# Kernel optimization log

Hardware: AMD Instinct MI355X
Metric: run time of the kernel (lower is better)

## Reference

```python
import jax, jax.numpy as jnp
import numpy as np

B, S, D, H, RANK, NC = 2, 2048, 1024, 16, 128, 16
DH = D // H


def setup_inputs() -> dict:
    key = jax.random.key(0)
    ks = jax.random.split(key, 10)
    x = jax.random.normal(ks[0], (B, S, D), jnp.float32)
    # causal mask, broadcast over batch and heads like torch's [B,1,S,S]
    mask = jnp.tril(jnp.ones((S, S), dtype=bool))[None, None]
    # orthogonal-ish init approximated by scaled gaussian
    compress_neurons = jax.random.normal(ks[1], (NC, D, RANK), jnp.float32) / np.sqrt(D)
    router_Q = jax.random.normal(ks[2], (NC, D), jnp.float32) * 0.02
    router_K = jax.random.normal(ks[3], (NC, D), jnp.float32) * 0.02
    router_V = jax.random.normal(ks[4], (NC, D), jnp.float32) * 0.02
    wQ = jax.random.normal(ks[5], (D, RANK), jnp.float32) / np.sqrt(RANK)
    wK = jax.random.normal(ks[6], (D, RANK), jnp.float32) / np.sqrt(RANK)
    wV = jax.random.normal(ks[7], (D, RANK), jnp.float32) / np.sqrt(RANK)
    wO = jax.random.normal(ks[8], (D, D), jnp.float32) / np.sqrt(D)
    return {"x": x, "mask": mask, "compress_neurons": compress_neurons,
            "router_Q": router_Q, "router_K": router_K, "router_V": router_V,
            "wQ": wQ, "wK": wK, "wV": wV, "wO": wO}


def reference(x, mask, compress_neurons, router_Q, router_K, router_V, wQ, wK, wV, wO):
    def compress(router_w):
        # router scores -> softmax over all n_compress neurons
        w = jax.nn.softmax(jnp.einsum('bsd,nd->bsn', x, router_w), axis=-1)  # [B,S,NC]
        # softmax-weighted sum of all neuron projections (fused einsum)
        return jnp.einsum('bsd,ndr,bsn->bsr', x, compress_neurons, w)  # [B,S,RANK]

    hQ = compress(router_Q)
    hK = compress(router_K)
    hV = compress(router_V)
    # expand rank -> d_model (Linear weight [D,RANK]), then split heads
    Q = jnp.einsum('bsr,dr->bsd', hQ, wQ).reshape(B, S, H, DH).transpose(0, 2, 1, 3)
    K = jnp.einsum('bsr,dr->bsd', hK, wK).reshape(B, S, H, DH).transpose(0, 2, 1, 3)
    V = jnp.einsum('bsr,dr->bsd', hV, wV).reshape(B, S, H, DH).transpose(0, 2, 1, 3)
    scores = jnp.einsum('bhqd,bhkd->bhqk', Q, K) / np.sqrt(DH)  # [B,H,S,S]
    scores = jnp.where(mask, scores, -jnp.inf)
    attn = jax.nn.softmax(scores, axis=-1)
    attn_out = jnp.einsum('bhqk,bhkd->bhqd', attn, V)
    attn_out = attn_out.transpose(0, 2, 1, 3).reshape(B, S, D)
    # dropout omitted (eval mode / dropout=0)
    return jnp.einsum('bsd,ed->bse', attn_out, wO)
```

## Files before the change

### kernel.cpp

```cpp
#include <hip/hip_runtime.h>
#include <hip/hip_bf16.h>
#include <math.h>

#define B_ 2
#define S_ 2048
#define D_ 1024
#define H_ 16
#define RANK_ 128
#define NC_ 16
#define DH_ 64
#define T_ (B_*S_)
#define NZ_ 2176

typedef __attribute__((ext_vector_type(8))) __bf16 bf16x8;
typedef __attribute__((ext_vector_type(8))) unsigned short u16x8;
typedef __attribute__((ext_vector_type(4))) float f32x4;
typedef __attribute__((ext_vector_type(16))) float f32x16;

#if __has_builtin(__builtin_amdgcn_exp2f)
#define EXP2F(x) __builtin_amdgcn_exp2f(x)
#else
#define EXP2F(x) exp2f(x)
#endif

__device__ __forceinline__ unsigned short f2bu(float f) {
    __hip_bfloat16 h = __float2bfloat16(f);
    unsigned short u; __builtin_memcpy(&u, &h, 2); return u;
}
__device__ __forceinline__ float bu2f(unsigned short u) {
    __hip_bfloat16 h; __builtin_memcpy(&h, &u, 2); return __bfloat162float(h);
}

__device__ __forceinline__ void gl_lds16(const unsigned short* g, unsigned short* l) {
    __builtin_amdgcn_global_load_lds(
        (const __attribute__((address_space(1))) void*)g,
        (__attribute__((address_space(3))) void*)l, 16, 0, 0);
}

__device__ __forceinline__ unsigned cvtpk_bf16(float lo, float hi) {
    unsigned r;
    asm("v_cvt_pk_bf16_f32 %0, %1, %2" : "=v"(r) : "v"(lo), "v"(hi));
    return r;
}
__device__ __forceinline__ void plswap(unsigned &a, unsigned &b) {
    asm("v_permlane32_swap_b32 %0, %1" : "+v"(a), "+v"(b));
}

__device__ __forceinline__ bool sniff_f32(const unsigned* __restrict__ p) {
    int votes = 0;
    #pragma unroll
    for (int i = 0; i < 64; i++) {
        unsigned e = (p[i] >> 23) & 0xFFu;
        votes += (e >= 0x60u && e <= 0x8Fu) ? 1 : 0;
    }
    return votes >= 32;
}

struct Cvt { const void* src[9]; unsigned short* dst[9]; const void* C; unsigned short* Ct; };

__global__ __launch_bounds__(256) void k_inputs(Cvt cv,
    const unsigned* __restrict__ probe)
{
    bool f32 = sniff_f32(probe);
    if (blockIdx.x < 512) {
        int bid = blockIdx.x;
        int d0 = (bid & 15) * 64, r0 = ((bid >> 4) & 1) * 64, n = bid >> 5;
        __shared__ unsigned short tile[64][65];
        for (int idx = threadIdx.x; idx < 4096; idx += 256) {
            int row = idx >> 6, col = idx & 63;
            size_t si = ((size_t)n*D_ + d0 + row)*RANK_ + r0 + col;
            tile[row][col] = f32 ? f2bu(((const float*)cv.C)[si])
                                 : ((const unsigned short*)cv.C)[si];
        }
        __syncthreads();
        for (int idx = threadIdx.x; idx < 4096; idx += 256) {
            int row = idx >> 6, col = idx & 63;
            cv.Ct[((size_t)(n*RANK_ + r0 + row))*D_ + d0 + col] = tile[col][row];
        }
        return;
    }
    const int offs[9] = {0, 4194304, 4210688, 4227072, 4243456,
                         4259840, 4390912, 4521984, 4653056};
    const int total = 5701632;
    int nconv = gridDim.x - 512;
    int stride = nconv * 256;
    for (int i = (blockIdx.x - 512) * 256 + threadIdx.x; i < total; i += stride) {
        int seg = 0;
        #pragma unroll
        for (int s = 1; s < 9; s++) seg += (i >= offs[s]) ? 1 : 0;
        int local = i - offs[seg];
        const void* sp = cv.src[seg];
        unsigned short v = 0;
        if (sp) v = f32 ? f2bu(((const float*)sp)[local]) : ((const unsigned short*)sp)[local];
        cv.dst[seg][local] = v;
    }
}

template<int MT, int MODE>
__global__ __launch_bounds__(256) void k_mfma_gemm(const unsigned short* __restrict__ A,
    const unsigned short* __restrict__ Bm, void* __restrict__ Cout,
    const unsigned* __restrict__ probe, int M, int N, int K)
{
    bool f32out = false;
    if (MODE == 2) f32out = sniff_f32(probe);
    __shared__ __align__(16) unsigned short As[MT*32*32];
    __shared__ __align__(16) unsigned short Bs[128*32];
    const int tid = threadIdx.x;
    const int wv = tid >> 6, lane = tid & 63;
    const int wm = (wv >> 1) * (MT*16), wn = (wv & 1) * 64;
    const int quad = lane >> 4, l16 = lane & 15;
    const int m0 = blockIdx.x * (MT*32), n0 = blockIdx.y * 128;

    const f32x4 z4 = {0.f, 0.f, 0.f, 0.f};
    f32x4 acc[MT][4];
    #pragma unroll
    for (int i = 0; i < MT; i++)
        #pragma unroll
        for (int j = 0; j < 4; j++) acc[i][j] = z4;

    for (int k0 = 0; k0 < K; k0 += 32) {
        __syncthreads();
        #pragma unroll
        for (int c = 0; c < MT/2; c++) {
            int idx = wv*64 + c*256 + lane;
            gl_lds16(A + (size_t)(m0 + (idx >> 2))*K + k0 + (idx & 3)*8,
                     &As[(wv*64 + c*256)*8]);
        }
        #pragma unroll
        for (int c = 0; c < 2; c++) {
            int idx = wv*64 + c*256 + lane;
            gl_lds16(Bm + (size_t)(n0 + (idx >> 2))*K + k0 + (idx & 3)*8,
                     &Bs[(wv*64 + c*256)*8]);
        }
        __syncthreads();
        bf16x8 af[MT], bfr[4];
        #pragma unroll
        for (int mt = 0; mt < MT; mt++) af[mt]  = *(const bf16x8*)&As[(wm + mt*16 + l16)*32 + quad*8];
        #pragma unroll
        for (int nt = 0; nt < 4; nt++) bfr[nt] = *(const bf16x8*)&Bs[(wn + nt*16 + l16)*32 + quad*8];
        #pragma unroll
        for (int mt = 0; mt < MT; mt++)
            #pragma unroll
            for (int nt = 0; nt < 4; nt++)
                acc[mt][nt] = __builtin_amdgcn_mfma_f32_16x16x32_bf16(af[mt], bfr[nt], acc[mt][nt], 0, 0, 0);
    }
    #pragma unroll
    for (int mt = 0; mt < MT; mt++)
        #pragma unroll
        for (int nt = 0; nt < 4; nt++) {
            int col = n0 + wn + nt*16 + l16;
            #pragma unroll
            for (int r = 0; r < 4; r++) {
                int rowg = m0 + wm + mt*16 + quad*4 + r;
                float v = acc[mt][nt][r];
                if (MODE == 2 && f32out) ((float*)Cout)[(size_t)rowg*N + col] = v;
                else  ((unsigned short*)Cout)[(size_t)rowg*N + col] = f2bu(v);
            }
        }
}

__global__ __launch_bounds__(256) void k_qkv2(const unsigned short* __restrict__ h3,
    const unsigned short* __restrict__ wqkv, unsigned short* __restrict__ QKb,
    unsigned short* __restrict__ Vtg)
{
    __shared__ __align__(16) unsigned short As[128*32];
    __shared__ __align__(16) unsigned short Bs[128*32];
    const int tid = threadIdx.x;
    const int wv = tid >> 6, lane = tid & 63;
    const int wm = (wv >> 1) * 64, wn = (wv & 1) * 64;
    const int quad = lane >> 4, l16 = lane & 15;

    const bool vt = (blockIdx.x >= 512);
    int m0, n0;
    const unsigned short *A, *Bm;
    float scale = 1.f;
    if (!vt) {
        int id = blockIdx.x;
        m0 = (id & 31) * 128;
        n0 = (id >> 5) * 128;
        int w = n0 >> 10;
        A  = h3 + (size_t)w * T_ * RANK_ + (size_t)m0 * RANK_;
        Bm = wqkv + (size_t)w * D_ * RANK_ + (size_t)(n0 & 1023) * RANK_;
        if (w == 0) scale = 0.125f * 1.44269504f;
    } else {
        int id = blockIdx.x - 512;
        m0 = (id & 7) * 128;
        n0 = (id >> 3) * 128;
        A  = wqkv + (size_t)2 * D_ * RANK_ + (size_t)m0 * RANK_;
        Bm = h3 + (size_t)2 * T_ * RANK_ + (size_t)n0 * RANK_;
    }

    const f32x4 z4 = {0.f, 0.f, 0.f, 0.f};
    f32x4 acc[4][4];
    #pragma unroll
    for (int i = 0; i < 4; i++)
        #pragma unroll
        for (int j = 0; j < 4; j++) acc[i][j] = z4;

    for (int k0 = 0; k0 < RANK_; k0 += 32) {
        __syncthreads();
        #pragma unroll
        for (int c = 0; c < 2; c++) {
            int idx = wv*64 + c*256 + lane;
            gl_lds16(A  + (size_t)(idx >> 2)*RANK_ + k0 + (idx & 3)*8,
                     &As[(wv*64 + c*256)*8]);
            gl_lds16(Bm + (size_t)(idx >> 2)*RANK_ + k0 + (idx & 3)*8,
                     &Bs[(wv*64 + c*256)*8]);
        }
        __syncthreads();
        bf16x8 af[4], bfr[4];
        #pragma unroll
        for (int mt = 0; mt < 4; mt++) af[mt]  = *(const bf16x8*)&As[(wm + mt*16 + l16)*32 + quad*8];
        #pragma unroll
        for (int nt = 0; nt < 4; nt++) bfr[nt] = *(const bf16x8*)&Bs[(wn + nt*16 + l16)*32 + quad*8];
        #pragma unroll
        for (int mt = 0; mt < 4; mt++)
            #pragma unroll
            for (int nt = 0; nt < 4; nt++)
                acc[mt][nt] = __builtin_amdgcn_mfma_f32_16x16x32_bf16(af[mt], bfr[nt], acc[mt][nt], 0, 0, 0);
    }
    #pragma unroll
    for (int mt = 0; mt < 4; mt++)
        #pragma unroll
        for (int nt = 0; nt < 4; nt++) {
            #pragma unroll
            for (int r = 0; r < 4; r++) {
                int rowg = m0 + wm + mt*16 + quad*4 + r;
                int col  = n0 + wn + nt*16 + l16;
                float v = acc[mt][nt][r] * scale;
                if (!vt) {
                    QKb[(size_t)(col >> 10)*T_*D_ + (size_t)rowg*D_ + (col & 1023)]
                        = f2bu(v);
                } else {
                    size_t vrow = (size_t)((col >> 11)*H_ + (rowg >> 6))*64 + (rowg & 63);
                    Vtg[vrow*S_ + (col & 2047)] = f2bu(v);
                }
            }
        }
}

__global__ __launch_bounds__(256) void k_hreduce(const unsigned short* __restrict__ z,
    unsigned short* __restrict__ h)
{
    int t0 = blockIdx.x * 2;
    int tg = threadIdx.x >> 7, r = threadIdx.x & 127;
    int t = t0 + tg;
    __shared__ float sc[2][48];
    __shared__ float wl[2][3][16];
    if (threadIdx.x < 96) {
        int tk = threadIdx.x / 48, j = threadIdx.x % 48;
        sc[tk][j] = bu2f(z[(size_t)(t0 + tk)*NZ_ + 2048 + j]);
    }
    __syncthreads();
    if (threadIdx.x < 6) {
        int tk = threadIdx.x / 3, w = threadIdx.x % 3;
        float m = -INFINITY;
        for (int n = 0; n < 16; n++) m = fmaxf(m, sc[tk][w*16 + n]);
        float s = 0.f, e[16];
        for (int n = 0; n < 16; n++) { e[n] = __expf(sc[tk][w*16 + n] - m); s += e[n]; }
        float inv = 1.f / s;
        for (int n = 0; n < 16; n++) wl[tk][w][n] = e[n] * inv;
    }
    __syncthreads();
    const unsigned short* zr = z + (size_t)t * NZ_;
    float acc[3] = {0.f, 0.f, 0.f};
    #pragma unroll
    for (int n = 0; n < NC_; n++) {
        float zv = bu2f(zr[n*RANK_ + r]);
        #pragma unroll
        for (int w = 0; w < 3; w++) acc[w] += wl[tg][w][n] * zv;
    }
    #pragma unroll
    for (int w = 0; w < 3; w++) h[((size_t)w*T_ + t)*RANK_ + r] = f2bu(acc[w]);
}

__global__ __launch_bounds__(256, 2) void k_flash_mfma(const unsigned short* __restrict__ Qm,
    const unsigned short* __restrict__ Km, const unsigned short* __restrict__ Vtg,
    unsigned short* __restrict__ Om)
{
    const int qt = 15 - blockIdx.x;
    const int hh = blockIdx.y, b = blockIdx.z;
    __shared__ __align__(16) unsigned short Ks[2][64*64];
    __shared__ __align__(16) unsigned short Vs[2][64*64];
    const int tid = threadIdx.x;
    const int w = tid >> 6, lane = tid & 63;
    const int l32 = lane & 31, hi = lane >> 5;
    const size_t base  = ((size_t)b * S_) * D_ + (size_t)hh * DH_;
    const size_t vbase = (size_t)((b*H_ + hh) * 64) * S_;
    const int tokg = qt*128 + w*32 + l32;

    bf16x8 aq[4];
    #pragma unroll
    for (int ks = 0; ks < 4; ks++)
        aq[ks] = *(const bf16x8*)(Qm + base + (size_t)tokg*D_ + ks*16 + hi*8);

    f32x16 oacc[2];
    #pragma unroll
    for (int db = 0; db < 2; db++)
        #pragma unroll
        for (int i = 0; i < 16; i++) oacc[db][i] = 0.f;
    float lsum = 0.f;

    const int nkt = 2*(qt + 1);

    #pragma unroll
    for (int c = 0; c < 2; c++) {
        int idx = c*256 + tid;
        int row = idx >> 3, j = (idx & 7) ^ (row & 7);
        gl_lds16(Km + base + (size_t)row*D_ + j*8, &Ks[0][(c*256 + (w<<6))*8]);
    }
    #pragma unroll
    for (int c = 0; c < 2; c++) {
        int idx = c*256 + tid;
        int row = idx >> 3, j = (idx & 7) ^ (row & 7);
        gl_lds16(Vtg + vbase + (size_t)row*S_ + j*8, &Vs[0][(c*256 + (w<<6))*8]);
    }

    for (int kt = 0; kt < nkt; kt++) {
        const int cur = kt & 1;
        __syncthreads();

        if (kt + 1 < nkt) {
            #pragma unroll
            for (int c = 0; c < 2; c++) {
                int idx = c*256 + tid;
                int row = idx >> 3, j = (idx & 7) ^ (row & 7);
                gl_lds16(Km + base + (size_t)((kt+1)*64 + row)*D_ + j*8,
                         &Ks[1-cur][(c*256 + (w<<6))*8]);
            }
            #pragma unroll
            for (int c = 0; c < 2; c++) {
                int idx = c*256 + tid;
                int row = idx >> 3, j = (idx & 7) ^ (row & 7);
                gl_lds16(Vtg + vbase + (size_t)row*S_ + (kt+1)*64 + j*8,
                         &Vs[1-cur][(c*256 + (w<<6))*8]);
            }
        }

        f32x16 sacc[2];
        #pragma unroll
        for (int kb = 0; kb < 2; kb++)
            #pragma unroll
            for (int i = 0; i < 16; i++) sacc[kb][i] = 0.f;
        #pragma unroll
        for (int ks = 0; ks < 4; ks++)
            #pragma unroll
            for (int kb = 0; kb < 2; kb++) {
                int row = kb*32 + l32;
                int c = (ks*2 + hi) ^ (row & 7);
                bf16x8 ak = *(const bf16x8*)&Ks[cur][row*64 + c*8];
                sacc[kb] = __builtin_amdgcn_mfma_f32_32x32x16_bf16(ak, aq[ks], sacc[kb], 0, 0, 0);
            }

        if (kt >= 2*qt) {
            #pragma unroll
            for (int kb = 0; kb < 2; kb++)
                #pragma unroll
                for (int r = 0; r < 16; r++) {
                    int keyg = kt*64 + kb*32 + (r&3) + 8*(r>>2) + 4*hi;
                    if (keyg > tokg) sacc[kb][r] = -INFINITY;
                }
        }

        bf16x8 pa[4];
        #pragma unroll
        for (int kb = 0; kb < 2; kb++) {
            float pv[16];
            #pragma unroll
            for (int r = 0; r < 16; r++) {
                pv[r] = EXP2F(sacc[kb][r]);
                lsum += pv[r];
            }
            unsigned wd[8];
            #pragma unroll
            for (int j = 0; j < 8; j++) wd[j] = cvtpk_bf16(pv[2*j], pv[2*j+1]);
            plswap(wd[0], wd[2]); plswap(wd[1], wd[3]);
            plswap(wd[4], wd[6]); plswap(wd[5], wd[7]);
            union { unsigned u[4]; bf16x8 v; } u0, u1;
            u0.u[0]=wd[0]; u0.u[1]=wd[1]; u0.u[2]=wd[2]; u0.u[3]=wd[3];
            u1.u[0]=wd[4]; u1.u[1]=wd[5]; u1.u[2]=wd[6]; u1.u[3]=wd[7];
            pa[2*kb]   = u0.v;
            pa[2*kb+1] = u1.v;
        }

        #pragma unroll
        for (int ks = 0; ks < 4; ks++)
            #pragma unroll
            for (int db = 0; db < 2; db++) {
                int row = db*32 + l32;
                int c = (ks*2 + hi) ^ (row & 7);
                bf16x8 bv = *(const bf16x8*)&Vs[cur][row*64 + c*8];
                oacc[db] = __builtin_amdgcn_mfma_f32_32x32x16_bf16(pa[ks], bv, oacc[db], 0, 0, 0);
            }
    }

    float l = lsum + __shfl_xor(lsum, 32);
    float inv = 1.f / l;
    #pragma unroll
    for (int r = 0; r < 16; r++) {
        int crow = (r&3) + 8*(r>>2) + 4*hi;
        float invr = __shfl(inv, crow);
        size_t rowo = base + (size_t)(qt*128 + w*32 + crow)*D_;
        #pragma unroll
        for (int db = 0; db < 2; db++)
            Om[rowo + db*32 + l32] = f2bu(oacc[db][r] * invr);
    }
}

extern "C" void kernel_launch(void* const* d_in, const int* in_sizes, int n_in,
                              void* d_out, int out_size, void* d_ws, size_t ws_size,
                              hipStream_t stream)
{
    const unsigned* probe = (const unsigned*)d_in[0];

    unsigned short* u = (unsigned short*)d_ws;
    unsigned short* xc   = u;               size_t o = (size_t)T_*D_;
    unsigned short* wqkv = u + o;           o += (size_t)3*D_*RANK_;
    unsigned short* wOc  = u + o;           o += (size_t)D_*D_;
    unsigned short* Ct   = u + o;           o += (size_t)NZ_*D_;
    unsigned short* h3   = u + o;           o += (size_t)3*T_*RANK_;
    unsigned short* QKb  = u + o;           o += (size_t)2*T_*D_;
    unsigned short* Vtg  = u + o;           o += (size_t)T_*D_;
    unsigned short* z    = u + o;           o += (size_t)T_*NZ_;
    unsigned short* attnb= u + o;           o += (size_t)T_*D_;

    unsigned short* Rp = Ct + (size_t)2048*D_;
    unsigned short* Qb = QKb;
    unsigned short* Kb = QKb + (size_t)T_*D_;

    Cvt cv;
    cv.src[0] = d_in[0]; cv.dst[0] = xc;
    cv.src[1] = d_in[3]; cv.dst[1] = Rp;
    cv.src[2] = d_in[4]; cv.dst[2] = Rp + 16384;
    cv.src[3] = d_in[5]; cv.dst[3] = Rp + 32768;
    cv.src[4] = nullptr; cv.dst[4] = Rp + 49152;
    cv.src[5] = d_in[6]; cv.dst[5] = wqkv;
    cv.src[6] = d_in[7]; cv.dst[6] = wqkv + 131072;
    cv.src[7] = d_in[8]; cv.dst[7] = wqkv + 262144;
    cv.src[8] = d_in[9]; cv.dst[8] = wOc;
    cv.C = d_in[2]; cv.Ct = Ct;
    k_inputs<<<512 + 2048, 256, 0, stream>>>(cv, probe);

    k_mfma_gemm<4,0><<<dim3(T_/128, NZ_/128), 256, 0, stream>>>(
        xc, Ct, z, nullptr, T_, NZ_, D_);

    k_hreduce<<<T_/2, 256, 0, stream>>>(z, h3);

    k_qkv2<<<768, 256, 0, stream>>>(h3, wqkv, QKb, Vtg);

    k_flash_mfma<<<dim3(16, H_, B_), 256, 0, stream>>>(Qb, Kb, Vtg, attnb);

    k_mfma_gemm<2,2><<<dim3(T_/64, D_/128), 256, 0, stream>>>(
        attnb, wOc, d_out, probe, T_, D_, D_);
}
```

Measured before the change: 233.6 us.

## Process two query tiles per wave in flash attention with 4-stage K/V pipeline

Each block in the attention kernel now covers 256 queries: every wave computes two 32-row query tiles against each staged K/V tile. This reuses each LDS K/V load for twice the MFMA work. The K/V double buffer becomes a 4-deep ring filled three tiles ahead, with explicit vmcnt waits and raw barriers replacing __syncthreads. The grid halves to 256 blocks with occupancy 1 and the reversed query-tile ordering is dropped, so causal load imbalance across blocks gets coarser and the heaviest blocks are no longer scheduled first.

```diff
diff --git a/kernel.cpp b/kernel.cpp
--- a/kernel.cpp
+++ b/kernel.cpp
@@ -274,74 +274,81 @@
     for (int w = 0; w < 3; w++) h[((size_t)w*T_ + t)*RANK_ + r] = f2bu(acc[w]);
 }
 
-__global__ __launch_bounds__(256, 2) void k_flash_mfma(const unsigned short* __restrict__ Qm,
+__global__ __launch_bounds__(256, 1) void k_flash_mfma(const unsigned short* __restrict__ Qm,
     const unsigned short* __restrict__ Km, const unsigned short* __restrict__ Vtg,
     unsigned short* __restrict__ Om)
 {
-    const int qt = 15 - blockIdx.x;
+    const int qt = blockIdx.x;
     const int hh = blockIdx.y, b = blockIdx.z;
-    __shared__ __align__(16) unsigned short Ks[2][64*64];
-    __shared__ __align__(16) unsigned short Vs[2][64*64];
+    __shared__ __align__(16) unsigned short Ks[4][64*64];
+    __shared__ __align__(16) unsigned short Vs[4][64*64];
     const int tid = threadIdx.x;
     const int w = tid >> 6, lane = tid & 63;
     const int l32 = lane & 31, hi = lane >> 5;
     const size_t base  = ((size_t)b * S_) * D_ + (size_t)hh * DH_;
     const size_t vbase = (size_t)((b*H_ + hh) * 64) * S_;
-    const int tokg = qt*128 + w*32 + l32;
-
-    bf16x8 aq[4];
-    #pragma unroll
-    for (int ks = 0; ks < 4; ks++)
-        aq[ks] = *(const bf16x8*)(Qm + base + (size_t)tokg*D_ + ks*16 + hi*8);
-
-    f32x16 oacc[2];
-    #pragma unroll
-    for (int db = 0; db < 2; db++)
-        #pragma unroll
-        for (int i = 0; i < 16; i++) oacc[db][i] = 0.f;
-    float lsum = 0.f;
-
-    const int nkt = 2*(qt + 1);
-
-    #pragma unroll
-    for (int c = 0; c < 2; c++) {
-        int idx = c*256 + tid;
-        int row = idx >> 3, j = (idx & 7) ^ (row & 7);
-        gl_lds16(Km + base + (size_t)row*D_ + j*8, &Ks[0][(c*256 + (w<<6))*8]);
-    }
-    #pragma unroll
-    for (int c = 0; c < 2; c++) {
-        int idx = c*256 + tid;
-        int row = idx >> 3, j = (idx & 7) ^ (row & 7);
-        gl_lds16(Vtg + vbase + (size_t)row*S_ + j*8, &Vs[0][(c*256 + (w<<6))*8]);
-    }
+    const int tok0 = qt*256 + w*64;
+
+    bf16x8 aq[2][4];
+    #pragma unroll
+    for (int tq = 0; tq < 2; tq++)
+        #pragma unroll
+        for (int ks = 0; ks < 4; ks++)
+            aq[tq][ks] = *(const bf16x8*)(Qm + base +
+                (size_t)(tok0 + tq*32 + l32)*D_ + ks*16 + hi*8);
+
+    const int nkt = 4*(qt + 1);
+
+    auto STAGE = [&](int kt_, int bf_) {
+        #pragma unroll
+        for (int c = 0; c < 2; c++) {
+            int idx = c*256 + tid;
+            int row = idx >> 3, j = (idx & 7) ^ (row & 7);
+            gl_lds16(Km + base + (size_t)(kt_*64 + row)*D_ + j*8,
+                     &Ks[bf_][(c*256 + (w<<6))*8]);
+        }
+        #pragma unroll
+        for (int c = 0; c < 2; c++) {
+            int idx = c*256 + tid;
+            int row = idx >> 3, j = (idx & 7) ^ (row & 7);
+            gl_lds16(Vtg + vbase + (size_t)row*S_ + kt_*64 + j*8,
+                     &Vs[bf_][(c*256 + (w<<6))*8]);
+        }
+    };
+
+    STAGE(0, 0); STAGE(1, 1); STAGE(2, 2);
+
+    f32x16 oacc[2][2];
+    #pragma unroll
+    for (int tq = 0; tq < 2; tq++)
+        #pragma unroll
+        for (int db = 0; db < 2; db++)
+            #pragma unroll
+            for (int i = 0; i < 16; i++) oacc[tq][db][i] = 0.f;
+    float ls[2][4];
+    #pragma unroll
+    for (int tq = 0; tq < 2; tq++)
+        #pragma unroll
+        for (int j = 0; j < 4; j++) ls[tq][j] = 0.f;
 
     for (int kt = 0; kt < nkt; kt++) {
-        const int cur = kt & 1;
-        __syncthreads();
-
-        if (kt + 1 < nkt) {
-            #pragma unroll
-            for (int c = 0; c < 2; c++) {
-                int idx = c*256 + tid;
-                int row = idx >> 3, j = (idx & 7) ^ (row & 7);
-                gl_lds16(Km + base + (size_t)((kt+1)*64 + row)*D_ + j*8,
-                         &Ks[1-cur][(c*256 + (w<<6))*8]);
-            }
-            #pragma unroll
-            for (int c = 0; c < 2; c++) {
-                int idx = c*256 + tid;
-                int row = idx >> 3, j = (idx & 7) ^ (row & 7);
-                gl_lds16(Vtg + vbase + (size_t)row*S_ + (kt+1)*64 + j*8,
-                         &Vs[1-cur][(c*256 + (w<<6))*8]);
-            }
-        }
-
-        f32x16 sacc[2];
-        #pragma unroll
-        for (int kb = 0; kb < 2; kb++)
-            #pragma unroll
-            for (int i = 0; i < 16; i++) sacc[kb][i] = 0.f;
+        const int cur = kt & 3;
+        const int rem = nkt - 1 - kt;
+        if (rem >= 2)      asm volatile("s_waitcnt vmcnt(8)" ::: "memory");
+        else if (rem == 1) asm volatile("s_waitcnt vmcnt(4)" ::: "memory");
+        else               asm volatile("s_waitcnt vmcnt(0)" ::: "memory");
+        __builtin_amdgcn_s_barrier();
+        __builtin_amdgcn_sched_barrier(0);
+
+        if (kt + 3 < nkt) STAGE(kt + 3, (kt + 3) & 3);
+
+        f32x16 sacc[2][2];
+        #pragma unroll
+        for (int tq = 0; tq < 2; tq++)
+            #pragma unroll
+            for (int kb = 0; kb < 2; kb++)
+                #pragma unroll
+                for (int i = 0; i < 16; i++) sacc[tq][kb][i] = 0.f;
         #pragma unroll
         for (int ks = 0; ks < 4; ks++)
             #pragma unroll
@@ -349,39 +356,46 @@
                 int row = kb*32 + l32;
                 int c = (ks*2 + hi) ^ (row & 7);
                 bf16x8 ak = *(const bf16x8*)&Ks[cur][row*64 + c*8];
-                sacc[kb] = __builtin_amdgcn_mfma_f32_32x32x16_bf16(ak, aq[ks], sacc[kb], 0, 0, 0);
-            }
-
-        if (kt >= 2*qt) {
-            #pragma unroll
-            for (int kb = 0; kb < 2; kb++)
+                sacc[0][kb] = __builtin_amdgcn_mfma_f32_32x32x16_bf16(ak, aq[0][ks], sacc[0][kb], 0, 0, 0);
+                sacc[1][kb] = __builtin_amdgcn_mfma_f32_32x32x16_bf16(ak, aq[1][ks], sacc[1][kb], 0, 0, 0);
+            }
+
+        if (kt >= 4*qt) {
+            #pragma unroll
+            for (int tq = 0; tq < 2; tq++) {
+                int tokg = tok0 + tq*32 + l32;
+                #pragma unroll
+                for (int kb = 0; kb < 2; kb++)
+                    #pragma unroll
+                    for (int r = 0; r < 16; r++) {
+                        int keyg = kt*64 + kb*32 + (r&3) + 8*(r>>2) + 4*hi;
+                        if (keyg > tokg) sacc[tq][kb][r] = -INFINITY;
+                    }
+            }
+        }
+
+        bf16x8 pa[2][4];
+        #pragma unroll
+        for (int tq = 0; tq < 2; tq++)
+            #pragma unroll
+            for (int kb = 0; kb < 2; kb++) {
+                float pv[16];
                 #pragma unroll
                 for (int r = 0; r < 16; r++) {
-                    int keyg = kt*64 + kb*32 + (r&3) + 8*(r>>2) + 4*hi;
-                    if (keyg > tokg) sacc[kb][r] = -INFINITY;
+                    pv[r] = EXP2F(sacc[tq][kb][r]);
+                    ls[tq][r & 3] += pv[r];
                 }
-        }
-
-        bf16x8 pa[4];
-        #pragma unroll
-        for (int kb = 0; kb < 2; kb++) {
-            float pv[16];
-            #pragma unroll
-            for (int r = 0; r < 16; r++) {
-                pv[r] = EXP2F(sacc[kb][r]);
-                lsum += pv[r];
-            }
-            unsigned wd[8];
-            #pragma unroll
-            for (int j = 0; j < 8; j++) wd[j] = cvtpk_bf16(pv[2*j], pv[2*j+1]);
-            plswap(wd[0], wd[2]); plswap(wd[1], wd[3]);
-            plswap(wd[4], wd[6]); plswap(wd[5], wd[7]);
-            union { unsigned u[4]; bf16x8 v; } u0, u1;
-            u0.u[0]=wd[0]; u0.u[1]=wd[1]; u0.u[2]=wd[2]; u0.u[3]=wd[3];
-            u1.u[0]=wd[4]; u1.u[1]=wd[5]; u1.u[2]=wd[6]; u1.u[3]=wd[7];
-            pa[2*kb]   = u0.v;
-            pa[2*kb+1] = u1.v;
-        }
+                unsigned wd[8];
+                #pragma unroll
+                for (int j = 0; j < 8; j++) wd[j] = cvtpk_bf16(pv[2*j], pv[2*j+1]);
+                plswap(wd[0], wd[2]); plswap(wd[1], wd[3]);
+                plswap(wd[4], wd[6]); plswap(wd[5], wd[7]);
+                union { unsigned u[4]; bf16x8 v; } u0, u1;
+                u0.u[0]=wd[0]; u0.u[1]=wd[1]; u0.u[2]=wd[2]; u0.u[3]=wd[3];
+                u1.u[0]=wd[4]; u1.u[1]=wd[5]; u1.u[2]=wd[6]; u1.u[3]=wd[7];
+                pa[tq][2*kb]   = u0.v;
+                pa[tq][2*kb+1] = u1.v;
+            }
 
         #pragma unroll
         for (int ks = 0; ks < 4; ks++)
@@ -390,20 +404,25 @@
                 int row = db*32 + l32;
                 int c = (ks*2 + hi) ^ (row & 7);
                 bf16x8 bv = *(const bf16x8*)&Vs[cur][row*64 + c*8];
-                oacc[db] = __builtin_amdgcn_mfma_f32_32x32x16_bf16(pa[ks], bv, oacc[db], 0, 0, 0);
-            }
-    }
-
-    float l = lsum + __shfl_xor(lsum, 32);
-    float inv = 1.f / l;
-    #pragma unroll
-    for (int r = 0; r < 16; r++) {
-        int crow = (r&3) + 8*(r>>2) + 4*hi;
-        float invr = __shfl(inv, crow);
-        size_t rowo = base + (size_t)(qt*128 + w*32 + crow)*D_;
-        #pragma unroll
-        for (int db = 0; db < 2; db++)
-            Om[rowo + db*32 + l32] = f2bu(oacc[db][r] * invr);
+                oacc[0][db] = __builtin_amdgcn_mfma_f32_32x32x16_bf16(pa[0][ks], bv, oacc[0][db], 0, 0, 0);
+                oacc[1][db] = __builtin_amdgcn_mfma_f32_32x32x16_bf16(pa[1][ks], bv, oacc[1][db], 0, 0, 0);
+            }
+    }
+
+    #pragma unroll
+    for (int tq = 0; tq < 2; tq++) {
+        float l = (ls[tq][0] + ls[tq][1]) + (ls[tq][2] + ls[tq][3]);
+        l += __shfl_xor(l, 32);
+        float inv = 1.f / l;
+        #pragma unroll
+        for (int r = 0; r < 16; r++) {
+            int crow = (r&3) + 8*(r>>2) + 4*hi;
+            float invr = __shfl(inv, crow);
+            size_t rowo = base + (size_t)(tok0 + tq*32 + crow)*D_;
+            #pragma unroll
+            for (int db = 0; db < 2; db++)
+                Om[rowo + db*32 + l32] = f2bu(oacc[tq][db][r] * invr);
+        }
     }
 }
 
@@ -448,7 +467,7 @@
 
     k_qkv2<<<768, 256, 0, stream>>>(h3, wqkv, QKb, Vtg);
 
-    k_flash_mfma<<<dim3(16, H_, B_), 256, 0, stream>>>(Qb, Kb, Vtg, attnb);
+    k_flash_mfma<<<dim3(8, H_, B_), 256, 0, stream>>>(Qb, Kb, Vtg, attnb);
 
     k_mfma_gemm<2,2><<<dim3(T_/64, D_/128), 256, 0, stream>>>(
         attnb, wOc, d_out, probe, T_, D_, D_);
```

Measured after the change: 255.2 us. 1.09x slower.
